# Performance work log

Hardware: AMD Instinct MI355X
Metric: run time of the kernel (lower is better)

Reference implementation:

```python
import jax, jax.numpy as jnp
import numpy as np
from jax import lax

B, C, HW = 8, 512, 32
NH = 8            # num_heads
NG = 32           # num_groups
HD = C // NH      # head_size = 64
EPS = 1e-6


def group_norm(x, gamma, beta, groups=NG, eps=EPS):
    b, c, h, w = x.shape
    xr = x.reshape(b, groups, c // groups, h, w)
    mu = xr.mean(axis=(2, 3, 4), keepdims=True)
    var = xr.var(axis=(2, 3, 4), keepdims=True)
    xn = ((xr - mu) / jnp.sqrt(var + eps)).reshape(b, c, h, w)
    return xn * gamma[None, :, None, None] + beta[None, :, None, None]


def conv2d(x, w, b):
    y = lax.conv_general_dilated(x, w, (1, 1), 'SAME',
                                 dimension_numbers=('NCHW', 'OIHW', 'NCHW'))
    return y + b[None, :, None, None]


def setup_inputs() -> dict:
    key = jax.random.key(0)
    ks = jax.random.split(key, 24)
    f32 = jnp.float32

    def lin(k, out_d, in_d):
        return (jax.random.normal(k, (out_d, in_d), f32) / np.sqrt(in_d)).astype(f32)

    inp = {
        'hidden_states': jax.random.normal(ks[0], (B, C, HW, HW), f32),
        'pre_g': jnp.ones(C, f32), 'pre_b': jnp.zeros(C, f32),
        'norm_g': jnp.ones(C, f32), 'norm_b': jnp.zeros(C, f32),
        'post_g': jnp.ones(C, f32), 'post_b': jnp.zeros(C, f32),
        'pos_emb': jax.random.normal(ks[1], (1, C, 32, 32), f32) * 0.02,
        'sa_w1': (jax.random.normal(ks[2], (C // 8, C, 1, 1), f32) / np.sqrt(C)),
        'sa_b1': jnp.zeros(C // 8, f32),
        'sa_w2': (jax.random.normal(ks[3], (C // 8, C // 8, 3, 3), f32) / np.sqrt(9 * C // 8)),
        'sa_b2': jnp.zeros(C // 8, f32),
        'sa_w3': (jax.random.normal(ks[4], (1, C // 8, 1, 1), f32) / np.sqrt(C // 8)),
        'sa_b3': jnp.zeros(1, f32),
        'wq': lin(ks[5], C, C), 'wk': lin(ks[6], C, C), 'wv': lin(ks[7], C, C),
        'wq0': lin(ks[8], C // 2, C), 'wk0': lin(ks[9], C // 2, C), 'wv0': lin(ks[10], C // 2, C),
        'wq1': lin(ks[11], C // 2, C), 'wk1': lin(ks[12], C // 2, C), 'wv1': lin(ks[13], C // 2, C),
        'ff_w1': lin(ks[14], C, 2 * C), 'ff_b1': jnp.zeros(C, f32),
        'ff_w2': lin(ks[15], C, C), 'ff_b2': jnp.zeros(C, f32),
        'out_w': lin(ks[16], C, C), 'out_b': jnp.zeros(C, f32),
    }
    return inp


def reference(hidden_states, pre_g, pre_b, norm_g, norm_b, post_g, post_b,
              pos_emb, sa_w1, sa_b1, sa_w2, sa_b2, sa_w3, sa_b3,
              wq, wk, wv, wq0, wk0, wv0, wq1, wk1, wv1,
              ff_w1, ff_b1, ff_w2, ff_b2, out_w, out_b):
    b, c, h, w = hidden_states.shape
    S = h * w
    residual = hidden_states

    hs = group_norm(hidden_states, pre_g, pre_b)
    # H=W=32 matches pos_embedding; bilinear resize to same size is identity
    hs = hs + pos_emb

    # spatial attention gating (conv 1x1 -> SiLU -> conv 3x3 -> SiLU -> conv 1x1 -> sigmoid)
    a = jax.nn.silu(conv2d(hs, sa_w1, sa_b1))
    a = jax.nn.silu(conv2d(a, sa_w2, sa_b2))
    spatial_weights = jax.nn.sigmoid(conv2d(a, sa_w3, sa_b3))
    spatial_enhanced = hs * spatial_weights

    # standard multi-head self-attention over flattened tokens
    sh = group_norm(hs, norm_g, norm_b).reshape(b, c, S).transpose(0, 2, 1)  # (B,S,C)
    ehs = sh  # encoder_hidden_states defaults to standard_hidden

    q = (sh @ wq.T).reshape(b, S, NH, HD)
    k = (ehs @ wk.T).reshape(b, S, NH, HD)
    v = (ehs @ wv.T).reshape(b, S, NH, HD)
    scores = jnp.einsum('bqhd,bkhd->bhqk', q, k) / np.sqrt(HD)
    probs = jax.nn.softmax(scores, axis=-1)
    std_out = jnp.einsum('bhqk,bkhd->bqhd', probs, v).reshape(b, S, c)

    # two multi-scale single-head attention branches (dim C/2 each)
    msh = spatial_enhanced.reshape(b, c, S).transpose(0, 2, 1)  # (B,S,C)
    parts = []
    for wqm, wkm, wvm in ((wq0, wk0, wv0), (wq1, wk1, wv1)):
        qm = msh @ wqm.T          # (B,S,C/2)
        km = ehs @ wkm.T
        vm = ehs @ wvm.T
        sc = jnp.einsum('bqd,bkd->bqk', qm, km) / np.sqrt(c // 2)
        parts.append(jnp.einsum('bqk,bkd->bqd', jax.nn.softmax(sc, axis=-1), vm))
    multi_out = jnp.concatenate(parts, axis=-1)  # (B,S,C)

    combined = jnp.concatenate([std_out, multi_out], axis=-1)  # (B,S,2C)
    fused = jax.nn.silu(combined @ ff_w1.T + ff_b1) @ ff_w2.T + ff_b2  # dropout = eval identity
    final = fused @ out_w.T + out_b
    final = final.transpose(0, 2, 1).reshape(b, c, h, w)
    final = group_norm(final, post_g, post_b)
    return final + residual
```

## Files before the change

### kernel.cpp

```cpp
#include <hip/hip_runtime.h>
#include <hip/hip_bf16.h>
#include <math.h>

typedef __attribute__((ext_vector_type(8))) __bf16 v8bf;
typedef __attribute__((ext_vector_type(4))) float v4f;

__device__ __forceinline__ unsigned short f2bf(float f) {
  union { float f; unsigned int u; } a; a.f = f;
  unsigned int r = a.u + 0x7fffu + ((a.u >> 16) & 1u);
  return (unsigned short)(r >> 16);
}
__device__ __forceinline__ unsigned short f2bf_trunc(float f) {
  union { float f; unsigned int u; } a; a.f = f;
  return (unsigned short)(a.u >> 16);
}
__device__ __forceinline__ float bf2f(unsigned short u) {
  union { unsigned int i; float f; } a; a.i = ((unsigned int)u) << 16; return a.f;
}
__device__ __forceinline__ float sigm(float x) { return 1.0f / (1.0f + __expf(-x)); }

__device__ __forceinline__ void async16(const void* g, void* l) {
  __builtin_amdgcn_global_load_lds(
      (const __attribute__((address_space(1))) unsigned int*)g,
      (__attribute__((address_space(3))) unsigned int*)l, 16, 0, 0);
}

__global__ __launch_bounds__(256) void gn_pre_kernel(
    const float* __restrict__ x, const float* __restrict__ g, const float* __restrict__ be,
    const float* __restrict__ pos, unsigned short* __restrict__ hsb, float* __restrict__ stats) {
  __shared__ float L[16384];
  __shared__ float rs[4], rs2[4], mr[2];
  int b = blockIdx.x >> 5, grp = blockIdx.x & 31;
  const float4* base = (const float4*)(x + ((size_t)b*512 + grp*16)*1024);
  float4* L4 = (float4*)L;
  int w = threadIdx.x >> 6;
  float s = 0.f, s2 = 0.f;
  for (int i = threadIdx.x; i < 4096; i += 256) {
    float4 v = base[i];
    L4[i] = v;
    s += v.x + v.y + v.z + v.w;
    s2 += v.x*v.x + v.y*v.y + v.z*v.z + v.w*v.w;
  }
#pragma unroll
  for (int o = 32; o; o >>= 1) { s += __shfl_xor(s, o); s2 += __shfl_xor(s2, o); }
  if ((threadIdx.x & 63) == 0) { rs[w] = s; rs2[w] = s2; }
  __syncthreads();
  if (threadIdx.x == 0) {
    float ts = rs[0]+rs[1]+rs[2]+rs[3], ts2 = rs2[0]+rs2[1]+rs2[2]+rs2[3];
    float mu = ts * (1.0f/16384.0f);
    float var = ts2 * (1.0f/16384.0f) - mu*mu;
    mr[0] = mu; mr[1] = rsqrtf(var + 1e-6f);
  }
  __syncthreads();
  float mu = mr[0], rstd = mr[1];
  const float4* pb = (const float4*)(pos + (size_t)grp*16*1024);
  float ns = 0.f, ns2 = 0.f;
  for (int i = threadIdx.x; i < 4096; i += 256) {
    float4 v = L4[i], p = pb[i];
    int c = grp*16 + (i >> 8);
    float gg = g[c], bb = be[c];
    float4 o;
    o.x = (v.x - mu)*rstd*gg + bb + p.x;
    o.y = (v.y - mu)*rstd*gg + bb + p.y;
    o.z = (v.z - mu)*rstd*gg + bb + p.z;
    o.w = (v.w - mu)*rstd*gg + bb + p.w;
    L4[i] = o;
    ns += o.x + o.y + o.z + o.w;
    ns2 += o.x*o.x + o.y*o.y + o.z*o.z + o.w*o.w;
  }
#pragma unroll
  for (int o = 32; o; o >>= 1) { ns += __shfl_xor(ns, o); ns2 += __shfl_xor(ns2, o); }
  if ((threadIdx.x & 63) == 0) { rs[w] = ns; rs2[w] = ns2; }
  __syncthreads();
  if (threadIdx.x == 0) {
    float ts = rs[0]+rs[1]+rs[2]+rs[3], ts2 = rs2[0]+rs2[1]+rs2[2]+rs2[3];
    float nmu = ts * (1.0f/16384.0f);
    float nvar = ts2 * (1.0f/16384.0f) - nmu*nmu;
    stats[(b*32+grp)*2] = nmu; stats[(b*32+grp)*2+1] = rsqrtf(nvar + 1e-6f);
  }
#pragma unroll
  for (int j = 0; j < 4; ++j) {
    int sI = threadIdx.x + j*256;
    unsigned int wd[8];
#pragma unroll
    for (int c = 0; c < 8; ++c) {
      unsigned int lo = f2bf(L[(2*c)*1024 + sI]);
      unsigned int hi = f2bf(L[(2*c+1)*1024 + sI]);
      wd[c] = lo | (hi << 16);
    }
    size_t oo = (size_t)(b*1024 + sI)*512 + grp*16;
    *(uint4*)(hsb + oo)     = make_uint4(wd[0], wd[1], wd[2], wd[3]);
    *(uint4*)(hsb + oo + 8) = make_uint4(wd[4], wd[5], wd[6], wd[7]);
  }
}

__global__ __launch_bounds__(256) void im2col_kernel(
    const unsigned short* __restrict__ a1, unsigned short* __restrict__ im2) {
  int row0 = blockIdx.x * 8;
#pragma unroll
  for (int it = 0; it < 3; ++it) {
    int cc = it*256 + threadIdx.x;
    if (cc >= 576) break;
    int rl = cc / 72, rr = cc - rl*72;
    int tap = rr >> 3, ch8 = rr & 7;
    int row = row0 + rl;
    int bb = row >> 10, s = row & 1023;
    int y = s >> 5, xx0 = s & 31;
    int yy = y + tap/3 - 1, xx = xx0 + tap%3 - 1;
    ushort4 v0 = make_ushort4(0,0,0,0), v1 = make_ushort4(0,0,0,0);
    if ((unsigned)yy < 32u && (unsigned)xx < 32u) {
      const unsigned short* src = a1 + ((size_t)(bb*1024 + yy*32 + xx))*64 + ch8*8;
      v0 = *(const ushort4*)src; v1 = *(const ushort4*)(src + 4);
    }
    unsigned short* dst = im2 + (size_t)row*576 + tap*64 + ch8*8;
    *(ushort4*)dst = v0; *(ushort4*)(dst + 4) = v1;
  }
}

__global__ __launch_bounds__(256) void gate_norm_kernel(
    const unsigned short* __restrict__ hsb, const unsigned short* __restrict__ a2,
    const float* __restrict__ w3, const float* __restrict__ b3,
    const float* __restrict__ stats, const float* __restrict__ g,
    const float* __restrict__ be,
    unsigned short* __restrict__ sh, unsigned short* __restrict__ msh) {
  int b = blockIdx.y;
  int s = blockIdx.x * 4 + (threadIdx.x >> 6);
  int oct = threadIdx.x & 63;
  int c0 = oct * 8;
  int grp = c0 >> 4;
  float part = bf2f(a2[((size_t)(b*1024) + s)*64 + oct]) * w3[oct];
#pragma unroll
  for (int o = 32; o; o >>= 1) part += __shfl_xor(part, o);
  float wgt = sigm(part + b3[0]);
  float mu = stats[(b*32 + grp)*2], rstd = stats[(b*32 + grp)*2 + 1];
  size_t o = (size_t)(b*1024 + s)*512 + c0;
  ushort4 u0 = *(const ushort4*)(hsb + o), u1 = *(const ushort4*)(hsb + o + 4);
  unsigned short uu[8] = {u0.x,u0.y,u0.z,u0.w,u1.x,u1.y,u1.z,u1.w};
  unsigned short so[8], mo[8];
#pragma unroll
  for (int j = 0; j < 8; ++j) {
    float v = bf2f(uu[j]);
    so[j] = f2bf((v - mu)*rstd*g[c0+j] + be[c0+j]);
    mo[j] = f2bf(v * wgt);
  }
  *(ushort4*)(sh + o)     = make_ushort4(so[0], so[1], so[2], so[3]);
  *(ushort4*)(sh + o + 4) = make_ushort4(so[4], so[5], so[6], so[7]);
  *(ushort4*)(msh + o)     = make_ushort4(mo[0], mo[1], mo[2], mo[3]);
  *(ushort4*)(msh + o + 4) = make_ushort4(mo[4], mo[5], mo[6], mo[7]);
}

struct WCvt { const float* src; int dstOff; int n; float scale; };
struct WCvtArgs { WCvt w[15]; };
__global__ __launch_bounds__(256) void wconvert_kernel(WCvtArgs a, unsigned short* __restrict__ dst) {
  WCvt e = a.w[blockIdx.y];
  int i = blockIdx.x * 256 + threadIdx.x;
  if (i >= e.n) return;
  if (blockIdx.y == 13) {
    int oc = i / 576, r = i - oc*576;
    int tap = r >> 6, ic = r & 63;
    dst[e.dstOff + i] = f2bf(e.src[(oc*64 + ic)*9 + tap]);
  } else if (blockIdx.y == 14) {
    dst[e.dstOff + i] = f2bf(e.src[(i & 511)*512 + (i >> 9)]);
  } else {
    dst[e.dstOff + i] = f2bf(e.src[i] * e.scale);
  }
}

__global__ __launch_bounds__(256) void bias_fold_kernel(
    const float* __restrict__ ow, const float* __restrict__ b2,
    const float* __restrict__ ob, float* __restrict__ bc) {
  int n = blockIdx.x * 256 + threadIdx.x;
  float s = ob[n];
  const float* r = ow + (size_t)n * 512;
#pragma unroll 8
  for (int j = 0; j < 512; ++j) s += r[j] * b2[j];
  bc[n] = s;
}

__global__ __launch_bounds__(256) void transpose2_kernel(
    const unsigned short* __restrict__ qkvm,
    unsigned short* __restrict__ vtb, unsigned short* __restrict__ vmt) {
  __shared__ unsigned short t[64][65];
  int s0 = blockIdx.x * 64, c0 = blockIdx.y * 64;
  int z = blockIdx.z, b = z & 7;
  const unsigned short* in = qkvm + (z >= 8 ? 2048 : 1024);
  unsigned short* out = (z >= 8) ? vmt : vtb;
  int tx = threadIdx.x & 63, ty = threadIdx.x >> 6;
#pragma unroll
  for (int i = 0; i < 16; ++i) {
    int s = ty + i*4;
    t[s][tx] = in[((size_t)(b*1024 + s0 + s))*2560 + c0 + tx];
  }
  __syncthreads();
#pragma unroll
  for (int i = 0; i < 16; ++i) {
    int c = ty + i*4;
    out[((size_t)b*512 + c0 + c)*1024 + s0 + tx] = t[tx][c];
  }
}

struct GemmDesc {
  const unsigned short* A; const unsigned short* B; void* out; const float* bias;
  int M, N, K, lda, ldb, ldo, epi;
  long long Ay, Az, By, Bz, Oy, Oz;
};

template<int BM, int BN>
__global__ __launch_bounds__(256) void gemm_tile_kernel(GemmDesc d) {
  constexpr int WGM = (BN >= 128) ? 2 : 4;
  constexpr int WGN = 4 / WGM;
  constexpr int MT = BM / (16 * WGM);
  constexpr int NT = BN / (16 * WGN);
  constexpr int AIT = (BM * 8) / 256;
  constexpr int BIT = (BN * 8) / 256;
  __shared__ __align__(16) unsigned short As[BM * 64];
  __shared__ __align__(16) unsigned short Bs[BN * 64];

  int ntx = d.N / BN, mtx = d.M / BM;
  int bmt, bnt;
  if ((mtx & 7) == 0) {
    int xcd = blockIdx.x & 7, j = blockIdx.x >> 3;
    int mpx = mtx >> 3;
    bmt = xcd * mpx + (j % mpx);
    bnt = j / mpx;
  } else {
    bmt = blockIdx.x / ntx; bnt = blockIdx.x % ntx;
  }
  int bm0 = bmt * BM, bn0 = bnt * BN;
  const unsigned short* A = d.A + (long long)blockIdx.y * d.Ay
      + (long long)blockIdx.z * d.Az + (size_t)bm0 * d.lda;
  const unsigned short* B = d.B + (long long)blockIdx.y * d.By
      + (long long)blockIdx.z * d.Bz + (size_t)bn0 * d.ldb;
  int tid = threadIdx.x, lane = tid & 63, w = tid >> 6;
  int wm = (WGN == 2) ? (w >> 1) : w;
  int wn = (WGN == 2) ? (w & 1) : 0;
  int ln = lane & 15, qd = lane >> 4;

  v4f acc[MT][NT];
#pragma unroll
  for (int i = 0; i < MT; ++i)
#pragma unroll
    for (int j = 0; j < NT; ++j) acc[i][j] = (v4f){0.f, 0.f, 0.f, 0.f};

  int nks = d.K >> 6;
  for (int ks = 0; ks < nks; ++ks) {
    int kof = ks * 64;
#pragma unroll
    for (int it = 0; it < AIT; ++it) {
      int c = it * 256 + tid;
      int row = c >> 3, ch = c & 7;
      async16(A + (size_t)row * d.lda + ((ch ^ (row & 7)) << 3) + kof, As + c * 8);
    }
#pragma unroll
    for (int it = 0; it < BIT; ++it) {
      int c = it * 256 + tid;
      int row = c >> 3, ch = c & 7;
      async16(B + (size_t)row * d.ldb + ((ch ^ (row & 7)) << 3) + kof, Bs + c * 8);
    }
    __syncthreads();
#pragma unroll
    for (int k2 = 0; k2 < 2; ++k2) {
      v8bf af[MT], bfr[NT];
#pragma unroll
      for (int i = 0; i < MT; ++i) {
        int row = wm * MT * 16 + i * 16 + ln;
        af[i] = *(const v8bf*)(As + row * 64 + (((k2*4 + qd) ^ (ln & 7)) << 3));
      }
#pragma unroll
      for (int j = 0; j < NT; ++j) {
        int row = wn * NT * 16 + j * 16 + ln;
        bfr[j] = *(const v8bf*)(Bs + row * 64 + (((k2*4 + qd) ^ (ln & 7)) << 3));
      }
#pragma unroll
      for (int i = 0; i < MT; ++i)
#pragma unroll
        for (int j = 0; j < NT; ++j)
          acc[i][j] = __builtin_amdgcn_mfma_f32_16x16x32_bf16(af[i], bfr[j], acc[i][j], 0, 0, 0);
    }
    __syncthreads();
  }

  size_t obase = (size_t)((long long)blockIdx.y * d.Oy + (long long)blockIdx.z * d.Oz);
#pragma unroll
  for (int i = 0; i < MT; ++i) {
#pragma unroll
    for (int j = 0; j < NT; ++j) {
      int col = bn0 + wn * NT * 16 + j * 16 + ln;
      float bia = d.bias ? d.bias[col] : 0.0f;
#pragma unroll
      for (int r = 0; r < 4; ++r) {
        int row = bm0 + wm * MT * 16 + i * 16 + qd * 4 + r;
        float v = acc[i][j][r] + bia;
        if (d.epi == 2) v = v * sigm(v);
        size_t oi = obase + (size_t)row * d.ldo + col;
        if (d.epi == 0) ((float*)d.out)[oi] = v;
        else ((unsigned short*)d.out)[oi] = f2bf(v);
      }
    }
  }
}

__global__ __launch_bounds__(512) void flash_attn_kernel(
    const unsigned short* __restrict__ QKVM, const unsigned short* __restrict__ VTB,
    unsigned short* __restrict__ out) {
  __shared__ __align__(16) unsigned short Ks[128*64];
  __shared__ __align__(16) unsigned short Vts[64*128];
  __shared__ __align__(16) unsigned short Pw[8][16*128];
  int h = blockIdx.x, b = blockIdx.y, qt = blockIdx.z;
  int tid = threadIdx.x, lane = tid & 63, w = tid >> 6;
  int ln = lane & 15, qd = lane >> 4;

  const unsigned short* Qbase = QKVM + ((size_t)(b*1024 + qt*128 + w*16))*2560 + h*64;
  v8bf aq[2];
#pragma unroll
  for (int s = 0; s < 2; ++s)
    aq[s] = *(const v8bf*)(Qbase + (size_t)ln*2560 + s*32 + qd*8);

  v4f o_acc[4];
  float l_part[4];
#pragma unroll
  for (int dn = 0; dn < 4; ++dn) o_acc[dn] = (v4f){0.f,0.f,0.f,0.f};
#pragma unroll
  for (int r = 0; r < 4; ++r) l_part[r] = 0.f;

  const unsigned short* Kg = QKVM + 512 + (size_t)(b*1024)*2560 + h*64;
  const unsigned short* Vg = VTB + ((size_t)(b*512) + h*64)*1024;

  for (int kt = 0; kt < 8; ++kt) {
#pragma unroll
    for (int it = 0; it < 2; ++it) {
      int c = it*512 + tid;
      async16(Kg + (size_t)(kt*128 + (c >> 3))*2560 + (((c & 7) ^ ((c >> 3) & 7)) << 3),
              Ks + c*8);
    }
#pragma unroll
    for (int it = 0; it < 2; ++it) {
      int c = it*512 + tid;
      async16(Vg + (size_t)(c >> 4)*1024 + kt*128 + ((((c & 15) ^ ((c >> 4) & 7))) << 3),
              Vts + c*8);
    }
    __syncthreads();

    v4f sc[8];
#pragma unroll
    for (int n = 0; n < 8; ++n) {
      v4f a = (v4f){0.f,0.f,0.f,0.f};
#pragma unroll
      for (int s = 0; s < 2; ++s) {
        v8bf kb = *(const v8bf*)(Ks + (n*16 + ln)*64 + (((s*4 + qd) ^ (ln & 7)) << 3));
        a = __builtin_amdgcn_mfma_f32_16x16x32_bf16(aq[s], kb, a, 0, 0, 0);
      }
      sc[n] = a;
    }
#pragma unroll
    for (int r = 0; r < 4; ++r) {
      int row7 = (qd*4 + r) & 7;
      float acc_l = 0.f;
#pragma unroll
      for (int n = 0; n < 8; ++n) {
        float p = exp2f(sc[n][r]);
        acc_l += p;
        Pw[w][(qd*4 + r)*128 + (((n*2 + (ln >> 3)) ^ row7) << 3) + (ln & 7)] = f2bf_trunc(p);
      }
      l_part[r] += acc_l;
    }
#pragma unroll
    for (int dn = 0; dn < 4; ++dn) {
      v4f a = o_acc[dn];
#pragma unroll
      for (int ks2 = 0; ks2 < 4; ++ks2) {
        int phys = (((ks2*4 + qd) ^ (ln & 7)) << 3);
        v8bf pf = *(const v8bf*)(&Pw[w][ln*128 + phys]);
        v8bf vf = *(const v8bf*)(Vts + (dn*16 + ln)*128 + phys);
        a = __builtin_amdgcn_mfma_f32_16x16x32_bf16(pf, vf, a, 0, 0, 0);
      }
      o_acc[dn] = a;
    }
    __syncthreads();
  }

  unsigned short* ob = out + ((size_t)(b*1024 + qt*128 + w*16))*1024 + h*64;
#pragma unroll
  for (int r = 0; r < 4; ++r) {
    float l = l_part[r];
    l += __shfl_xor(l, 1); l += __shfl_xor(l, 2);
    l += __shfl_xor(l, 4); l += __shfl_xor(l, 8);
    float rinv = 1.0f / l;
#pragma unroll
    for (int dn = 0; dn < 4; ++dn)
      ob[(size_t)(qd*4 + r)*1024 + dn*16 + ln] = f2bf(o_acc[dn][r] * rinv);
  }
}

__global__ __launch_bounds__(256) void softmax_bf16_kernel(
    const unsigned short* __restrict__ S, unsigned short* __restrict__ P, int nrows) {
  int row = blockIdx.x * 4 + (threadIdx.x >> 6);
  if (row >= nrows) return;
  int l = threadIdx.x & 63;
  const ushort4* sp = (const ushort4*)(S + (size_t)row * 1024);
  float v[16];
  float m = -1e30f;
#pragma unroll
  for (int t = 0; t < 4; ++t) {
    ushort4 u = sp[t*64 + l];
    v[t*4+0] = bf2f(u.x); v[t*4+1] = bf2f(u.y); v[t*4+2] = bf2f(u.z); v[t*4+3] = bf2f(u.w);
    m = fmaxf(m, fmaxf(fmaxf(v[t*4], v[t*4+1]), fmaxf(v[t*4+2], v[t*4+3])));
  }
#pragma unroll
  for (int o = 32; o; o >>= 1) m = fmaxf(m, __shfl_xor(m, o));
  float sum = 0.f;
#pragma unroll
  for (int t = 0; t < 16; ++t) { v[t] = __expf(v[t] - m); sum += v[t]; }
#pragma unroll
  for (int o = 32; o; o >>= 1) sum += __shfl_xor(sum, o);
  float r = 1.0f / sum;
  ushort4* p = (ushort4*)(P + (size_t)row * 1024);
#pragma unroll
  for (int t = 0; t < 4; ++t)
    p[t*64 + l] = make_ushort4(f2bf_trunc(v[t*4]*r), f2bf_trunc(v[t*4+1]*r),
                               f2bf_trunc(v[t*4+2]*r), f2bf_trunc(v[t*4+3]*r));
}

__global__ __launch_bounds__(256) void gn_stats_bf16_kernel(
    const unsigned short* __restrict__ t, float* __restrict__ stats) {
  int b = blockIdx.x >> 5, grp = blockIdx.x & 31;
  float s = 0.f, s2 = 0.f;
#pragma unroll
  for (int j = 0; j < 4; ++j) {
    int sI = threadIdx.x + j*256;
    const unsigned short* p = t + ((size_t)(b*1024 + sI))*512 + grp*16;
    uint4 a = *(const uint4*)p, c2 = *(const uint4*)(p + 8);
    unsigned int ww[8] = {a.x,a.y,a.z,a.w,c2.x,c2.y,c2.z,c2.w};
#pragma unroll
    for (int k = 0; k < 8; ++k) {
      float lo = bf2f((unsigned short)(ww[k] & 0xffff));
      float hi = bf2f((unsigned short)(ww[k] >> 16));
      s += lo + hi; s2 += lo*lo + hi*hi;
    }
  }
#pragma unroll
  for (int o = 32; o; o >>= 1) { s += __shfl_xor(s, o); s2 += __shfl_xor(s2, o); }
  __shared__ float rs[4], rs2[4];
  int w = threadIdx.x >> 6;
  if ((threadIdx.x & 63) == 0) { rs[w] = s; rs2[w] = s2; }
  __syncthreads();
  if (threadIdx.x == 0) {
    float ts = rs[0]+rs[1]+rs[2]+rs[3], ts2 = rs2[0]+rs2[1]+rs2[2]+rs2[3];
    float mu = ts * (1.0f/16384.0f);
    float var = ts2 * (1.0f/16384.0f) - mu*mu;
    stats[(b*32+grp)*2] = mu; stats[(b*32+grp)*2+1] = rsqrtf(var + 1e-6f);
  }
}

__global__ __launch_bounds__(256) void final_out_kernel(
    const unsigned short* __restrict__ fin, const float* __restrict__ stats,
    const float* __restrict__ g, const float* __restrict__ be,
    const float* __restrict__ x, float* __restrict__ out) {
  __shared__ float t[64][65];
  int s0 = blockIdx.x * 64, c0 = blockIdx.y * 64, b = blockIdx.z;
  int tx = threadIdx.x & 63, ty = threadIdx.x >> 6;
#pragma unroll
  for (int i = 0; i < 16; ++i) {
    int s = ty + i*4;
    t[s][tx] = bf2f(fin[((size_t)(b*1024 + s0 + s))*512 + c0 + tx]);
  }
  __syncthreads();
#pragma unroll
  for (int i = 0; i < 16; ++i) {
    int c = ty + i*4;
    int cc = c0 + c, grp = cc >> 4;
    float mu = stats[(b*32+grp)*2], rstd = stats[(b*32+grp)*2+1];
    float gg = g[cc], bb = be[cc];
    size_t oi = ((size_t)(b*512 + cc))*1024 + s0 + tx;
    out[oi] = (t[tx][c] - mu)*rstd*gg + bb + x[oi];
  }
}

static void launch_gemm128(hipStream_t st, const unsigned short* A, const unsigned short* B,
                           void* out, const float* bias,
                           int M, int N, int K, int lda, int ldb, int ldo, int epi,
                           long long Ay, long long Az, long long By, long long Bz,
                           long long Oy, long long Oz, int gy, int gz) {
  GemmDesc d{A, B, out, bias, M, N, K, lda, ldb, ldo, epi, Ay, Az, By, Bz, Oy, Oz};
  gemm_tile_kernel<128,128><<<dim3((M/128)*(N/128), gy, gz), dim3(256), 0, st>>>(d);
}
static void launch_gemm64(hipStream_t st, const unsigned short* A, const unsigned short* B,
                          void* out, const float* bias,
                          int M, int N, int K, int lda, int ldb, int ldo, int epi) {
  GemmDesc d{A, B, out, bias, M, N, K, lda, ldb, ldo, epi, 0,0,0,0,0,0};
  gemm_tile_kernel<128,64><<<dim3((M/128)*(N/64), 1, 1), dim3(256), 0, st>>>(d);
}

extern "C" void kernel_launch(void* const* d_in, const int* in_sizes, int n_in,
                              void* d_out, int out_size, void* d_ws, size_t ws_size,
                              hipStream_t stream) {
  const float* x      = (const float*)d_in[0];
  const float* pre_g  = (const float*)d_in[1];
  const float* pre_b  = (const float*)d_in[2];
  const float* norm_g = (const float*)d_in[3];
  const float* norm_b = (const float*)d_in[4];
  const float* post_g = (const float*)d_in[5];
  const float* post_b = (const float*)d_in[6];
  const float* pos    = (const float*)d_in[7];
  const float* sa_b1  = (const float*)d_in[9];
  const float* sa_b2  = (const float*)d_in[11];
  const float* sa_w3  = (const float*)d_in[12];
  const float* sa_b3  = (const float*)d_in[13];
  const float* ff_b1  = (const float*)d_in[24];
  const float* ff_b2  = (const float*)d_in[26];
  const float* out_w  = (const float*)d_in[27];
  const float* out_b  = (const float*)d_in[28];
  float* outp = (float*)d_out;

  char* ws = (char*)d_ws;
  size_t off = 0;
  auto alloc = [&](size_t bytes) -> void* {
    void* p = ws + off; off += (bytes + 255) & ~(size_t)255; return p;
  };
  float* STATS = (float*)alloc(4096);
  float* BC    = (float*)alloc(2048);
  unsigned short* HSB  = (unsigned short*)alloc(8388608);
  unsigned short* A1   = (unsigned short*)alloc(1048576);
  unsigned short* IM2  = (unsigned short*)alloc(9437184);
  unsigned short* A2   = (unsigned short*)alloc(1048576);
  unsigned short* SHB  = (unsigned short*)alloc(8388608);
  unsigned short* MSHB = (unsigned short*)alloc(8388608);
  unsigned short* WBF  = (unsigned short*)alloc(6291456);
  unsigned short* WCOMB= (unsigned short*)alloc(524288);
  unsigned short* QKVM = (unsigned short*)alloc(41943040);
  unsigned short* QM   = (unsigned short*)alloc(8388608);
  unsigned short* VTB  = (unsigned short*)alloc(8388608);
  unsigned short* VMT  = (unsigned short*)alloc(8388608);
  unsigned short* SBUF = (unsigned short*)alloc(33554432);
  unsigned short* PBUF = (unsigned short*)alloc(33554432);
  unsigned short* COMB = (unsigned short*)alloc(16777216);
  unsigned short* FFMID= (unsigned short*)alloc(8388608);
  unsigned short* FINALB=(unsigned short*)alloc(8388608);

  const int OQKVM=0, OQM=1310720, OFF1=1572864, OFF2T=2097152,
            OOW=2359296, OW1=2621440, OW2R=2654208;

  gn_pre_kernel<<<dim3(256), dim3(256), 0, stream>>>(x, pre_g, pre_b, pos, HSB, STATS);
  {
    WCvtArgs a;
    const float LG2E = 1.4426950408889634f;
    const int   srcIdx[15] = {14,15,16, 18,21,19,22, 17,20, 23,27, 8, 0, 10, 25};
    const int   dofs[15]   = {0, 262144, 524288,
                              786432, 917504, 1048576, 1179648,
                              OQM, OQM+131072,
                              OFF1, OOW, OW1, 0, OW2R, OFF2T};
    const int   ns[15]     = {262144,262144,262144, 131072,131072,131072,131072,
                              131072,131072, 524288,262144, 32768, 0, 36864, 262144};
    const float sc[15]     = {0.125f*LG2E,1.f,1.f, 1.f,1.f,1.f,1.f,
                              0.0625f,0.0625f, 1.f,1.f, 1.f, 0.f, 1.f, 1.f};
    for (int i = 0; i < 15; ++i) { a.w[i].src = (const float*)d_in[srcIdx[i]]; a.w[i].dstOff = dofs[i]; a.w[i].n = ns[i]; a.w[i].scale = sc[i]; }
    wconvert_kernel<<<dim3(2048, 15), dim3(256), 0, stream>>>(a, WBF);
  }
  {
    GemmDesc d{WBF+OOW, WBF+OFF2T, WCOMB, nullptr, 512, 512, 512, 512, 512, 512, 1, 0,0,0,0,0,0};
    gemm_tile_kernel<128,128><<<dim3(16, 1, 1), dim3(256), 0, stream>>>(d);
  }
  bias_fold_kernel<<<dim3(2), dim3(256), 0, stream>>>(out_w, ff_b2, out_b, BC);
  launch_gemm64(stream, HSB, WBF+OW1,  A1, sa_b1, 8192, 64, 512, 512, 512, 64, 2);
  im2col_kernel<<<dim3(1024), dim3(256), 0, stream>>>(A1, IM2);
  launch_gemm64(stream, IM2, WBF+OW2R, A2, sa_b2, 8192, 64, 576, 576, 576, 64, 2);
  gate_norm_kernel<<<dim3(256, 8), dim3(256), 0, stream>>>(HSB, A2, sa_w3, sa_b3, STATS, norm_g, norm_b, SHB, MSHB);

  launch_gemm128(stream, SHB,  WBF+OQKVM, QKVM, nullptr, 8192, 2560, 512, 512, 512, 2560, 1, 0,0,0,0,0,0, 1,1);
  launch_gemm64(stream, MSHB, WBF+OQM,   QM,   nullptr, 8192, 512,  512, 512, 512, 512,  1);

  transpose2_kernel<<<dim3(16, 8, 16), dim3(256), 0, stream>>>(QKVM, VTB, VMT);

  flash_attn_kernel<<<dim3(8, 8, 8), dim3(512), 0, stream>>>(QKVM, VTB, COMB);

  launch_gemm128(stream, QM, QKVM + 1536, SBUF, nullptr,
                 1024, 1024, 256, 512, 2560, 1024, 1,
                 1024LL*512, 256, 1024LL*2560, 256, 1024LL*1024, 8388608, 8, 2);
  softmax_bf16_kernel<<<dim3(4096), dim3(256), 0, stream>>>(SBUF, PBUF, 16384);
  launch_gemm128(stream, PBUF, VMT, COMB + 512, nullptr,
                 1024, 256, 1024, 1024, 1024, 1024, 1,
                 1024LL*1024, 8388608, 512LL*1024, 256LL*1024, 1024LL*1024, 256, 8, 2);

  launch_gemm64(stream, COMB,  WBF+OFF1, FFMID,  ff_b1, 8192, 512, 1024, 1024, 1024, 512, 2);
  launch_gemm64(stream, FFMID, WCOMB,    FINALB, BC,    8192, 512, 512,  512,  512,  512, 1);

  gn_stats_bf16_kernel<<<dim3(256), dim3(256), 0, stream>>>(FINALB, STATS);
  final_out_kernel<<<dim3(16, 8, 8), dim3(256), 0, stream>>>(FINALB, STATS, post_g, post_b, x, outp);

  (void)in_sizes; (void)n_in; (void)out_size; (void)ws_size;
}
```

Measured before the change: 406.7 us.

## Fuse multi-scale branch attention into a single flash-style kernel

Replaces the score GEMM, the separate bf16 softmax kernel and the probs·V GEMM of the two single-head multi-scale branches with one fused kernel. Each block keeps Q fragments in registers and streams swizzled K and Vᵀ tiles into LDS. It computes exp2 scores and accumulates unnormalized outputs plus row sums, then normalizes at the end. This removes the 32 MB score and probability buffers and their global-memory round trips, along with two kernel launches. The softmax folds log2e into the Q weight scale and skips max subtraction, so it relies on scores staying small enough not to overflow. The grid is only 256 blocks with large LDS use and no double buffering, which limits latency hiding.

```diff
diff --git a/kernel.cpp b/kernel.cpp
--- a/kernel.cpp
+++ b/kernel.cpp
@@ -392,33 +392,98 @@
   }
 }
 
-__global__ __launch_bounds__(256) void softmax_bf16_kernel(
-    const unsigned short* __restrict__ S, unsigned short* __restrict__ P, int nrows) {
-  int row = blockIdx.x * 4 + (threadIdx.x >> 6);
-  if (row >= nrows) return;
-  int l = threadIdx.x & 63;
-  const ushort4* sp = (const ushort4*)(S + (size_t)row * 1024);
-  float v[16];
-  float m = -1e30f;
-#pragma unroll
-  for (int t = 0; t < 4; ++t) {
-    ushort4 u = sp[t*64 + l];
-    v[t*4+0] = bf2f(u.x); v[t*4+1] = bf2f(u.y); v[t*4+2] = bf2f(u.z); v[t*4+3] = bf2f(u.w);
-    m = fmaxf(m, fmaxf(fmaxf(v[t*4], v[t*4+1]), fmaxf(v[t*4+2], v[t*4+3])));
-  }
-#pragma unroll
-  for (int o = 32; o; o >>= 1) m = fmaxf(m, __shfl_xor(m, o));
-  float sum = 0.f;
-#pragma unroll
-  for (int t = 0; t < 16; ++t) { v[t] = __expf(v[t] - m); sum += v[t]; }
-#pragma unroll
-  for (int o = 32; o; o >>= 1) sum += __shfl_xor(sum, o);
-  float r = 1.0f / sum;
-  ushort4* p = (ushort4*)(P + (size_t)row * 1024);
-#pragma unroll
-  for (int t = 0; t < 4; ++t)
-    p[t*64 + l] = make_ushort4(f2bf_trunc(v[t*4]*r), f2bf_trunc(v[t*4+1]*r),
-                               f2bf_trunc(v[t*4+2]*r), f2bf_trunc(v[t*4+3]*r));
+__global__ __launch_bounds__(256) void flash_branch_kernel(
+    const unsigned short* __restrict__ QKVM, const unsigned short* __restrict__ QM,
+    const unsigned short* __restrict__ VMT, unsigned short* __restrict__ out) {
+  __shared__ __align__(16) unsigned short Ks[64*256];
+  __shared__ __align__(16) unsigned short Vts[256*64];
+  __shared__ __align__(16) unsigned short Pw[4][16*64];
+  int bb = blockIdx.x, b = bb >> 1, br = bb & 1;
+  int qt = blockIdx.z;
+  int tid = threadIdx.x, lane = tid & 63, w = tid >> 6;
+  int ln = lane & 15, qd = lane >> 4;
+
+  const unsigned short* Qb = QM + ((size_t)(b*1024 + qt*64 + w*16))*512 + br*256;
+  v8bf aq[8];
+#pragma unroll
+  for (int s = 0; s < 8; ++s)
+    aq[s] = *(const v8bf*)(Qb + (size_t)ln*512 + s*32 + qd*8);
+
+  v4f o_acc[16];
+  float l_part[4];
+#pragma unroll
+  for (int dn = 0; dn < 16; ++dn) o_acc[dn] = (v4f){0.f,0.f,0.f,0.f};
+#pragma unroll
+  for (int r = 0; r < 4; ++r) l_part[r] = 0.f;
+
+  const unsigned short* Kg = QKVM + 1536 + br*256 + (size_t)(b*1024)*2560;
+  const unsigned short* Vg = VMT + ((size_t)(b*512) + br*256)*1024;
+
+  for (int kt = 0; kt < 16; ++kt) {
+#pragma unroll
+    for (int it = 0; it < 8; ++it) {
+      int c = it*256 + tid;
+      int row = c >> 5, ch = c & 31;
+      async16(Kg + (size_t)(kt*64 + row)*2560 + ((ch ^ (row & 7)) << 3), Ks + c*8);
+    }
+#pragma unroll
+    for (int it = 0; it < 8; ++it) {
+      int c = it*256 + tid;
+      int row = c >> 3, ch = c & 7;
+      async16(Vg + (size_t)row*1024 + kt*64 + ((ch ^ (row & 7)) << 3), Vts + c*8);
+    }
+    __syncthreads();
+
+    v4f sc[4];
+#pragma unroll
+    for (int n = 0; n < 4; ++n) {
+      v4f a = (v4f){0.f,0.f,0.f,0.f};
+      int krow = n*16 + ln;
+#pragma unroll
+      for (int s = 0; s < 8; ++s) {
+        v8bf kb = *(const v8bf*)(Ks + krow*256 + (((s*4 + qd) ^ (krow & 7)) << 3));
+        a = __builtin_amdgcn_mfma_f32_16x16x32_bf16(aq[s], kb, a, 0, 0, 0);
+      }
+      sc[n] = a;
+    }
+#pragma unroll
+    for (int r = 0; r < 4; ++r) {
+      int row7 = (qd*4 + r) & 7;
+      float acc_l = 0.f;
+#pragma unroll
+      for (int n = 0; n < 4; ++n) {
+        float p = exp2f(sc[n][r]);
+        acc_l += p;
+        Pw[w][(qd*4 + r)*64 + (((n*2 + (ln >> 3)) ^ row7) << 3) + (ln & 7)] = f2bf_trunc(p);
+      }
+      l_part[r] += acc_l;
+    }
+#pragma unroll
+    for (int dn = 0; dn < 16; ++dn) {
+      v4f a = o_acc[dn];
+#pragma unroll
+      for (int ks2 = 0; ks2 < 2; ++ks2) {
+        int phys = (((ks2*4 + qd) ^ (ln & 7)) << 3);
+        v8bf pf = *(const v8bf*)(&Pw[w][ln*64 + phys]);
+        v8bf vf = *(const v8bf*)(Vts + (dn*16 + ln)*64 + phys);
+        a = __builtin_amdgcn_mfma_f32_16x16x32_bf16(pf, vf, a, 0, 0, 0);
+      }
+      o_acc[dn] = a;
+    }
+    __syncthreads();
+  }
+
+  unsigned short* ob = out + ((size_t)(b*1024 + qt*64 + w*16))*1024 + 512 + br*256;
+#pragma unroll
+  for (int r = 0; r < 4; ++r) {
+    float l = l_part[r];
+    l += __shfl_xor(l, 1); l += __shfl_xor(l, 2);
+    l += __shfl_xor(l, 4); l += __shfl_xor(l, 8);
+    float rinv = 1.0f / l;
+#pragma unroll
+    for (int dn = 0; dn < 16; ++dn)
+      ob[(size_t)(qd*4 + r)*1024 + dn*16 + ln] = f2bf(o_acc[dn][r] * rinv);
+  }
 }
 
 __global__ __launch_bounds__(256) void gn_stats_bf16_kernel(
@@ -531,8 +596,6 @@
   unsigned short* QM   = (unsigned short*)alloc(8388608);
   unsigned short* VTB  = (unsigned short*)alloc(8388608);
   unsigned short* VMT  = (unsigned short*)alloc(8388608);
-  unsigned short* SBUF = (unsigned short*)alloc(33554432);
-  unsigned short* PBUF = (unsigned short*)alloc(33554432);
   unsigned short* COMB = (unsigned short*)alloc(16777216);
   unsigned short* FFMID= (unsigned short*)alloc(8388608);
   unsigned short* FINALB=(unsigned short*)alloc(8388608);
@@ -552,7 +615,7 @@
     const int   ns[15]     = {262144,262144,262144, 131072,131072,131072,131072,
                               131072,131072, 524288,262144, 32768, 0, 36864, 262144};
     const float sc[15]     = {0.125f*LG2E,1.f,1.f, 1.f,1.f,1.f,1.f,
-                              0.0625f,0.0625f, 1.f,1.f, 1.f, 0.f, 1.f, 1.f};
+                              0.0625f*LG2E,0.0625f*LG2E, 1.f,1.f, 1.f, 0.f, 1.f, 1.f};
     for (int i = 0; i < 15; ++i) { a.w[i].src = (const float*)d_in[srcIdx[i]]; a.w[i].dstOff = dofs[i]; a.w[i].n = ns[i]; a.w[i].scale = sc[i]; }
     wconvert_kernel<<<dim3(2048, 15), dim3(256), 0, stream>>>(a, WBF);
   }
@@ -573,13 +636,7 @@
 
   flash_attn_kernel<<<dim3(8, 8, 8), dim3(512), 0, stream>>>(QKVM, VTB, COMB);
 
-  launch_gemm128(stream, QM, QKVM + 1536, SBUF, nullptr,
-                 1024, 1024, 256, 512, 2560, 1024, 1,
-                 1024LL*512, 256, 1024LL*2560, 256, 1024LL*1024, 8388608, 8, 2);
-  softmax_bf16_kernel<<<dim3(4096), dim3(256), 0, stream>>>(SBUF, PBUF, 16384);
-  launch_gemm128(stream, PBUF, VMT, COMB + 512, nullptr,
-                 1024, 256, 1024, 1024, 1024, 1024, 1,
-                 1024LL*1024, 8388608, 512LL*1024, 256LL*1024, 1024LL*1024, 256, 8, 2);
+  flash_branch_kernel<<<dim3(16, 1, 16), dim3(256), 0, stream>>>(QKVM, QM, VMT, COMB);
 
   launch_gemm64(stream, COMB,  WBF+OFF1, FFMID,  ff_b1, 8192, 512, 1024, 1024, 1024, 512, 2);
   launch_gemm64(stream, FFMID, WCOMB,    FINALB, BC,    8192, 512, 512,  512,  512,  512, 1);
```

Measured after the change: 384.7 us (median of 2 runs). 5.4% less time.
